# Kernel tuning notes

Hardware: AMD Instinct MI355X
Metric: run time of the kernel (lower is better)

## Reference

```python
import jax, jax.numpy as jnp
import numpy as np

N, E = 50000, 400000
NS, NV = 16, 8      # node irreps: 16x0e + 8x1o
ES, EV = 8, 8       # edge irreps: 8x0e + 8x1o
HS, HV = 32, 16     # hidden: 32x0e gated-scalar outputs, 16x1o vectors (gated by 16 extra scalars)
HT = HS + HV        # total scalar channels produced by the TP (incl. gate scalars) = 48
OS, OV = 16, 8      # output irreps: 16x0e + 8x1o


def setup_inputs() -> dict:
    key = jax.random.key(0)
    ks = jax.random.split(key, 32)
    n = lambda i, shp: jax.random.normal(ks[i], shp, dtype=jnp.float32)
    return dict(
        node_s=n(0, (N, NS)), node_v=n(1, (N, NV, 3)), pos=n(2, (N, 3)),
        edge_s=n(3, (E, ES)), edge_v=n(4, (E, EV, 3)),
        edge_index=jax.random.randint(ks[5], (2, E), 0, N, dtype=jnp.int32),
        # tp_messages stage 1: node x node -> node-sized intermediate (trilinear TP split in two)
        W1ss=n(6, (NS, NS, NS)), W1sv=n(7, (NS, NV, NV)), W1vs=n(8, (NV, NS, NV)),
        W1vvs=n(9, (NV, NV, NS)), W1vvv=n(10, (NV, NV, NV)),
        # tp_messages stage 2: intermediate x edge_attr -> hidden
        W2ss=n(11, (NS, ES, HT)), W2sv=n(12, (NS, EV, HV)), W2vs=n(13, (NV, ES, HV)),
        W2vvs=n(14, (NV, EV, HT)), W2vvv=n(15, (NV, EV, HV)),
        # lin_messages_out (per-l equivariant linear)
        Lms=n(16, (HS, OS)), Lmv=n(17, (HV, OV)),
        # tp_update: node x aggregated -> hidden
        W3ss=n(18, (NS, OS, HT)), W3sv=n(19, (NS, OV, HV)), W3vs=n(20, (NV, OS, HV)),
        W3vvs=n(21, (NV, OV, HT)), W3vvv=n(22, (NV, OV, HV)),
        # lin_update_out
        Lus=n(23, (HS, OS)), Luv=n(24, (HV, OV)),
    )


def fctp(s1, v1, s2, v2, Wss, Wsv, Wvs, Wvvs, Wvvv):
    """FullyConnectedTensorProduct restricted to l<=1 irreps.
    Paths: 0x0->0, 1x1->0 (dot), 0x1->1, 1x0->1, 1x1->1 (cross).
    Each path normalized by sqrt(fan_in); multi-path outputs by sqrt(n_paths)."""
    m1s, m2s = s1.shape[1], s2.shape[1]
    m1v, m2v = v1.shape[1], v2.shape[1]
    i2, i3 = 1.0 / np.sqrt(2.0), 1.0 / np.sqrt(3.0)
    so = jnp.einsum('ei,ej,ijk->ek', s1, s2, Wss) / np.sqrt(m1s * m2s)
    so = so + jnp.einsum('eic,ejc,ijk->ek', v1, v2, Wvvs) * (i3 / np.sqrt(m1v * m2v))
    so = so * i2
    vo = jnp.einsum('ei,ejc,ijk->ekc', s1, v2, Wsv) / np.sqrt(m1s * m2v)
    vo = vo + jnp.einsum('eic,ej,ijk->ekc', v1, s2, Wvs) / np.sqrt(m1v * m2s)
    cr = jnp.cross(v1[:, :, None, :], v2[:, None, :, :])  # [E, m1v, m2v, 3]
    vo = vo + jnp.einsum('eijc,ijk->ekc', cr, Wvvv) * (i2 / np.sqrt(m1v * m2v))
    return so, vo * i3


def gate(s, v):
    """e3nn Gate: first HS scalars silu-activated, last HV scalars sigmoid-gate the vectors."""
    hg = v.shape[1]
    return jax.nn.silu(s[:, :-hg]), v * jax.nn.sigmoid(s[:, -hg:])[:, :, None]


def lin(s, v, Ws, Wv):
    """Per-l equivariant Linear with 1/sqrt(fan_in) normalization."""
    return (s @ Ws) / np.sqrt(s.shape[1]), jnp.einsum('eic,ij->ejc', v, Wv) / np.sqrt(v.shape[1])


def reference(node_s, node_v, pos, edge_s, edge_v, edge_index,
              W1ss, W1sv, W1vs, W1vvs, W1vvv,
              W2ss, W2sv, W2vs, W2vvs, W2vvv, Lms, Lmv,
              W3ss, W3sv, W3vs, W3vvs, W3vvv, Lus, Luv):
    n_nodes = node_s.shape[0]
    row, col = edge_index[0], edge_index[1]
    # messages: trilinear TP(x_row, x_col, edge_attr) -> hidden, then gate, then linear
    ms, mv = fctp(node_s[row], node_v[row], node_s[col], node_v[col],
                  W1ss, W1sv, W1vs, W1vvs, W1vvv)
    ms, mv = fctp(ms, mv, edge_s, edge_v, W2ss, W2sv, W2vs, W2vvs, W2vvv)
    ms, mv = gate(ms, mv)
    ms, mv = lin(ms, mv, Lms, Lmv)
    # scatter-sum aggregation over destination nodes (col), dim_size = N
    agg_s = jax.ops.segment_sum(ms, col, num_segments=n_nodes)
    agg_v = jax.ops.segment_sum(mv, col, num_segments=n_nodes)
    # update: TP(node, aggregated) -> hidden, gate, linear
    us, uv = fctp(node_s, node_v, agg_s, agg_v, W3ss, W3sv, W3vs, W3vvs, W3vvv)
    us, uv = gate(us, uv)
    us, uv = lin(us, uv, Lus, Luv)
    # concatenate irreps blocks into a single [N, OS + 3*OV] feature array
    return jnp.concatenate([us, uv.reshape(n_nodes, -1)], axis=1)
```

## Files before the change

kernel.cpp:

```cpp
#include <hip/hip_runtime.h>
#include <math.h>

typedef _Float16 half8 __attribute__((ext_vector_type(8)));
typedef float floatx4 __attribute__((ext_vector_type(4)));

constexpr float C_SS16 = 0.04419417382415922f;
constexpr float C_UNI  = 0.05103103630798288f;
constexpr float C2_SS  = 0.0625f;
constexpr float C2_VS  = 0.07216878364870323f;
constexpr float C_LS   = 0.17677669529663687f;
constexpr float C_LV   = 0.25f;
constexpr float RS     = 2048.0f;
constexpr float RSI    = 1.0f / 2048.0f;

__device__ __forceinline__ void split8s(const float* p, half8& ah, half8& alS) {
#pragma unroll
    for (int j = 0; j < 8; ++j) {
        _Float16 h = (_Float16)p[j];
        ah[j] = h;
        alS[j] = (_Float16)((p[j] - (float)h) * RS);
    }
}
__device__ __forceinline__ void mfma_tri(half8 ah, half8 alS, half8 bh, half8 blS,
                                         floatx4& acc, floatx4& accR) {
    acc  = __builtin_amdgcn_mfma_f32_16x16x32_f16(ah,  bh,  acc,  0, 0, 0);
    accR = __builtin_amdgcn_mfma_f32_16x16x32_f16(alS, bh,  accR, 0, 0, 0);
    accR = __builtin_amdgcn_mfma_f32_16x16x32_f16(ah,  blS, accR, 0, 0, 0);
}

__global__ void prep_w(const float* __restrict__ W1ss, const float* __restrict__ W1sv,
                       const float* __restrict__ W1vs, const float* __restrict__ W1vvs,
                       const float* __restrict__ W1vvv,
                       const float* __restrict__ W2ss, const float* __restrict__ W2sv,
                       const float* __restrict__ W2vs, const float* __restrict__ W2vvs,
                       const float* __restrict__ W2vvv,
                       const float* __restrict__ W3ss, const float* __restrict__ W3sv,
                       const float* __restrict__ W3vs, const float* __restrict__ W3vvs,
                       const float* __restrict__ W3vvv,
                       _Float16* B1sh, _Float16* B1sl, _Float16* B1vh, _Float16* B1vl,
                       _Float16* B2sh, _Float16* B2sl, _Float16* B2vh, _Float16* B2vl,
                       _Float16* B3sh, _Float16* B3sl, _Float16* B3vh, _Float16* B3vl)
{
    const int tid = threadIdx.x;
    for (int idx = tid; idx < 10*512; idx += 256) {
        int t_k = idx >> 9, lane = (idx >> 3) & 63, j = idx & 7;
        int q = lane >> 4, n = lane & 15;
        int k = t_k*32 + q*8 + j;
        float v;
        if (k < 256) { int i = k>>4, jj = k&15; v = W1ss[(i*16+jj)*16+n] * C_SS16; }
        else { int kk = k-256; int i = kk>>3, jj = kk&7; v = W1vvs[(i*8+jj)*16+n] * C_UNI; }
        _Float16 h = (_Float16)v;
        B1sh[idx] = h; B1sl[idx] = (_Float16)((v - (float)h) * RS);
    }
    for (int idx = tid; idx < 10*512; idx += 256) {
        int t_k = idx >> 9, lane = (idx >> 3) & 63, j = idx & 7;
        int q = lane >> 4, n = lane & 15;
        int k = t_k*32 + q*8 + j;
        float v = 0.f;
        if (n < 8) {
            if (k < 128) { int i = k>>3, jj = k&7; v = W1sv[(i*8+jj)*8+n] * C_UNI; }
            else if (k < 256) { int kk = k-128; int i = kk>>4, jj = kk&15; v = W1vs[(i*16+jj)*8+n] * C_UNI; }
            else { int kk = k-256; int i = kk>>3, jj = kk&7; v = W1vvv[(i*8+jj)*8+n] * C_UNI; }
        }
        _Float16 h = (_Float16)v;
        B1vh[idx] = h; B1vl[idx] = (_Float16)((v - (float)h) * RS);
    }
    for (int idx = tid; idx < 3*6*512; idx += 256) {
        int tn = idx / 3072, t_k = (idx % 3072) >> 9, lane = (idx >> 3) & 63, j = idx & 7;
        int q = lane >> 4, n = lane & 15, col = tn*16 + n;
        int k = t_k*32 + q*8 + j;
        float v;
        if (k < 128) { int i = k>>3, jj = k&7; v = W2ss[(i*8+jj)*48+col] * C2_SS; }
        else { int kk = k-128; int i = kk>>3, jj = kk&7; v = W2vvs[(i*8+jj)*48+col] * C_UNI; }
        _Float16 h = (_Float16)v;
        B2sh[idx] = h; B2sl[idx] = (_Float16)((v - (float)h) * RS);
    }
    for (int idx = tid; idx < 8*512; idx += 256) {
        int t_k = idx >> 9, lane = (idx >> 3) & 63, j = idx & 7;
        int q = lane >> 4, n = lane & 15;
        int k = t_k*32 + q*8 + j;
        float v;
        if (k < 128) { int i = k>>3, jj = k&7; v = W2sv[(i*8+jj)*16+n] * C_UNI; }
        else if (k < 192) { int kk = k-128; int i = kk>>3, jj = kk&7; v = W2vs[(i*8+jj)*16+n] * C2_VS; }
        else { int kk = k-192; int i = kk>>3, jj = kk&7; v = W2vvv[(i*8+jj)*16+n] * C_UNI; }
        _Float16 h = (_Float16)v;
        B2vh[idx] = h; B2vl[idx] = (_Float16)((v - (float)h) * RS);
    }
    for (int idx = tid; idx < 3*10*512; idx += 256) {
        int tn = idx / 5120, rem = idx % 5120;
        int t_k = rem >> 9, lane = (rem >> 3) & 63, j = rem & 7;
        int q = lane >> 4, n = lane & 15, col = tn*16 + n;
        int k = t_k*32 + q*8 + j;
        float v;
        if (k < 256) { int i = k>>4, jj = k&15; v = W3ss[(i*16+jj)*48+col] * C_SS16; }
        else { int kk = k-256; int i = kk>>3, jj = kk&7; v = W3vvs[(i*8+jj)*48+col] * C_UNI; }
        _Float16 h = (_Float16)v;
        B3sh[idx] = h; B3sl[idx] = (_Float16)((v - (float)h) * RS);
    }
    for (int idx = tid; idx < 10*512; idx += 256) {
        int t_k = idx >> 9, lane = (idx >> 3) & 63, j = idx & 7;
        int q = lane >> 4, n = lane & 15;
        int k = t_k*32 + q*8 + j;
        float v;
        if (k < 128) { int i = k>>3, jj = k&7; v = W3sv[(i*8+jj)*16+n] * C_UNI; }
        else if (k < 256) { int kk = k-128; int i = kk>>4, jj = kk&15; v = W3vs[(i*16+jj)*16+n] * C_UNI; }
        else { int kk = k-256; int i = kk>>3, jj = kk&7; v = W3vvv[(i*8+jj)*16+n] * C_UNI; }
        _Float16 h = (_Float16)v;
        B3vh[idx] = h; B3vl[idx] = (_Float16)((v - (float)h) * RS);
    }
}

__global__ __launch_bounds__(256)
void edge_fused(const float* __restrict__ ns, const float* __restrict__ nv,
                const float* __restrict__ edge_s, const float* __restrict__ edge_v,
                const int* __restrict__ ei,
                const _Float16* __restrict__ B1sh, const _Float16* __restrict__ B1sl,
                const _Float16* __restrict__ B1vh, const _Float16* __restrict__ B1vl,
                const _Float16* __restrict__ B2sh, const _Float16* __restrict__ B2sl,
                const _Float16* __restrict__ B2vh, const _Float16* __restrict__ B2vl,
                const float* __restrict__ Lms, const float* __restrict__ Lmv,
                float* __restrict__ m2h, int E)
{
    __shared__ float mT[4][16*41];
    __shared__ float ep[4][2][16*49];
    const int lane = threadIdx.x & 63;
    const int wv = threadIdx.x >> 6;
    const int e0 = (blockIdx.x*4 + wv) * 16;
    const int q = lane >> 4, n = lane & 15;
    const int e = min(e0 + n, E - 1);
    const int qh = q >> 1, ql = q & 1;
    const int r = ei[e], c2 = ei[E + e];

    float rs_sel[8], rs4[4], rva[2][3], rvs[4][3], csh[8], cv[8][3];
#pragma unroll
    for (int t = 0; t < 8; ++t) rs_sel[t] = ns[(size_t)r*16 + 2*t + qh];
#pragma unroll
    for (int t = 0; t < 4; ++t) rs4[t] = ns[(size_t)r*16 + 4*t + q];
#pragma unroll
    for (int cc = 0; cc < 3; ++cc) {
        rva[0][cc] = nv[(size_t)r*24 + 3*q + cc];
        rva[1][cc] = nv[(size_t)r*24 + 3*(q+4) + cc];
    }
#pragma unroll
    for (int u = 0; u < 4; ++u)
#pragma unroll
        for (int cc = 0; cc < 3; ++cc) rvs[u][cc] = nv[(size_t)r*24 + 3*(2*u+qh) + cc];
    {
        const float4* p = (const float4*)(ns + (size_t)c2*16 + ql*8);
#pragma unroll
        for (int t = 0; t < 2; ++t) { float4 v = p[t]; csh[4*t]=v.x; csh[4*t+1]=v.y; csh[4*t+2]=v.z; csh[4*t+3]=v.w; }
        const float4* pv = (const float4*)(nv + (size_t)c2*24);
        float tmp[24];
#pragma unroll
        for (int t = 0; t < 6; ++t) { float4 v = pv[t]; tmp[4*t]=v.x; tmp[4*t+1]=v.y; tmp[4*t+2]=v.z; tmp[4*t+3]=v.w; }
#pragma unroll
        for (int k = 0; k < 8; ++k) { cv[k][0]=tmp[3*k]; cv[k][1]=tmp[3*k+1]; cv[k][2]=tmp[3*k+2]; }
    }

    const half8* B1sH = (const half8*)B1sh; const half8* B1sL = (const half8*)B1sl;
    const half8* B1vH = (const half8*)B1vh; const half8* B1vL = (const half8*)B1vl;

    {
        floatx4 acc = {0.f,0.f,0.f,0.f}, accR = {0.f,0.f,0.f,0.f};
#pragma unroll
        for (int t = 0; t < 10; ++t) {
            float p[8];
            if (t < 8) {
                const float m = rs_sel[t];
#pragma unroll
                for (int j = 0; j < 8; ++j) p[j] = m * csh[j];
            } else {
                const int u = t - 8;
                const float vx = rva[u][0], vy = rva[u][1], vz = rva[u][2];
#pragma unroll
                for (int j = 0; j < 8; ++j) p[j] = fmaf(vx, cv[j][0], fmaf(vy, cv[j][1], vz*cv[j][2]));
            }
            half8 ah, al; split8s(p, ah, al);
            mfma_tri(ah, al, B1sH[t*64 + lane], B1sL[t*64 + lane], acc, accR);
        }
#pragma unroll
        for (int r2 = 0; r2 < 4; ++r2)
            mT[wv][(q*4 + r2)*41 + n] = acc[r2] + accR[r2]*RSI;
    }
#pragma unroll 1
    for (int c = 0; c < 3; ++c) {
        const int c1 = (c+1)%3, c2i = (c+2)%3;
        floatx4 acc = {0.f,0.f,0.f,0.f}, accR = {0.f,0.f,0.f,0.f};
#pragma unroll
        for (int t = 0; t < 10; ++t) {
            float p[8];
            if (t < 4) {
                const float m = rs4[t];
#pragma unroll
                for (int j = 0; j < 8; ++j) p[j] = m * cv[j][c];
            } else if (t < 8) {
                const float m = rvs[t-4][c];
#pragma unroll
                for (int j = 0; j < 8; ++j) p[j] = m * csh[j];
            } else {
                const int u = t - 8;
                const float v1 = rva[u][c1], v2 = rva[u][c2i];
#pragma unroll
                for (int j = 0; j < 8; ++j) p[j] = v1*cv[j][c2i] - v2*cv[j][c1];
            }
            half8 ah, al; split8s(p, ah, al);
            mfma_tri(ah, al, B1vH[t*64 + lane], B1vL[t*64 + lane], acc, accR);
        }
        if (n < 8) {
#pragma unroll
            for (int r2 = 0; r2 < 4; ++r2)
                mT[wv][(q*4 + r2)*41 + 16 + 3*n + c] = acc[r2] + accR[r2]*RSI;
        }
    }
    __syncthreads();

    float msr[4], mva[2][3], es[8], ev[8][3];
#pragma unroll
    for (int t = 0; t < 4; ++t) msr[t] = mT[wv][n*41 + 4*t + q];
#pragma unroll
    for (int u = 0; u < 2; ++u)
#pragma unroll
        for (int cc = 0; cc < 3; ++cc) mva[u][cc] = mT[wv][n*41 + 16 + 3*(4*u+q) + cc];
    {
        const float4* p = (const float4*)(edge_s + (size_t)e*8);
#pragma unroll
        for (int t = 0; t < 2; ++t) { float4 v = p[t]; es[4*t]=v.x; es[4*t+1]=v.y; es[4*t+2]=v.z; es[4*t+3]=v.w; }
        const float4* pv = (const float4*)(edge_v + (size_t)e*24);
        float tmp[24];
#pragma unroll
        for (int t = 0; t < 6; ++t) { float4 v = pv[t]; tmp[4*t]=v.x; tmp[4*t+1]=v.y; tmp[4*t+2]=v.z; tmp[4*t+3]=v.w; }
#pragma unroll
        for (int k = 0; k < 8; ++k) { ev[k][0]=tmp[3*k]; ev[k][1]=tmp[3*k+1]; ev[k][2]=tmp[3*k+2]; }
    }

    const half8* B2sH = (const half8*)B2sh; const half8* B2sL = (const half8*)B2sl;
    const half8* B2vH = (const half8*)B2vh; const half8* B2vL = (const half8*)B2vl;

    floatx4 accs[3], accsR[3];
#pragma unroll
    for (int t = 0; t < 3; ++t) { accs[t] = (floatx4){0.f,0.f,0.f,0.f}; accsR[t] = (floatx4){0.f,0.f,0.f,0.f}; }
#pragma unroll
    for (int t = 0; t < 6; ++t) {
        float p[8];
        if (t < 4) {
            const float m = msr[t];
#pragma unroll
            for (int j = 0; j < 8; ++j) p[j] = m * es[j];
        } else {
            const int u = t - 4;
            const float vx = mva[u][0], vy = mva[u][1], vz = mva[u][2];
#pragma unroll
            for (int j = 0; j < 8; ++j) p[j] = fmaf(vx, ev[j][0], fmaf(vy, ev[j][1], vz*ev[j][2]));
        }
        half8 ah, al; split8s(p, ah, al);
#pragma unroll
        for (int tn = 0; tn < 3; ++tn)
            mfma_tri(ah, al, B2sH[(tn*6 + t)*64 + lane], B2sL[(tn*6 + t)*64 + lane], accs[tn], accsR[tn]);
    }

    float* hsL = &ep[wv][0][0];
    float* gvL = &ep[wv][1][0];
#pragma unroll
    for (int t = 0; t < 3; ++t)
#pragma unroll
        for (int r2 = 0; r2 < 4; ++r2) {
            const int row = q*4 + r2;
            const float v = accs[t][r2] + accsR[t][r2]*RSI;
            if (t < 2) hsL[row*49 + t*16 + n] = v / (1.f + __expf(-v)) * C_LS;
            else       hsL[row*49 + 32 + n] = v;
        }
    __syncthreads();

    {
        float os[4] = {0.f, 0.f, 0.f, 0.f};
#pragma unroll 4
        for (int s = 0; s < 32; ++s) {
            const float hv_ = hsL[n*49 + s];
            const float4 w = *(const float4*)(Lms + s*16 + 4*q);
            os[0] = fmaf(hv_, w.x, os[0]); os[1] = fmaf(hv_, w.y, os[1]);
            os[2] = fmaf(hv_, w.z, os[2]); os[3] = fmaf(hv_, w.w, os[3]);
        }
        if (e0 + n < E) {
#pragma unroll
            for (int u = 0; u < 4; ++u)
                m2h[(size_t)(e0 + n)*40 + 4*q + u] = os[u];
        }
    }

    floatx4 accv[3];
#pragma unroll 1
    for (int c = 0; c < 3; ++c) {
        const int c1 = (c+1)%3, c2i = (c+2)%3;
        floatx4 acc = {0.f,0.f,0.f,0.f}, accR = {0.f,0.f,0.f,0.f};
#pragma unroll
        for (int t = 0; t < 8; ++t) {
            float p[8];
            if (t < 4) {
                const float m = msr[t];
#pragma unroll
                for (int j = 0; j < 8; ++j) p[j] = m * ev[j][c];
            } else if (t < 6) {
                const float m = mva[t-4][c];
#pragma unroll
                for (int j = 0; j < 8; ++j) p[j] = m * es[j];
            } else {
                const int u = t - 6;
                const float v1 = mva[u][c1], v2 = mva[u][c2i];
#pragma unroll
                for (int j = 0; j < 8; ++j) p[j] = v1*ev[j][c2i] - v2*ev[j][c1];
            }
            half8 ah, al; split8s(p, ah, al);
            mfma_tri(ah, al, B2vH[t*64 + lane], B2vL[t*64 + lane], acc, accR);
        }
#pragma unroll
        for (int r2 = 0; r2 < 4; ++r2) acc[r2] = acc[r2] + accR[r2]*RSI;
        accv[c] = acc;
    }
#pragma unroll
    for (int r2 = 0; r2 < 4; ++r2) {
        const int row = q*4 + r2;
        const float gt = C_LV / (1.f + __expf(-hsL[row*49 + 32 + n]));
#pragma unroll
        for (int c = 0; c < 3; ++c) gvL[row*49 + c*16 + n] = accv[c][r2] * gt;
    }
    __syncthreads();

    {
        float ov[3][2] = {{0.f,0.f},{0.f,0.f},{0.f,0.f}};
#pragma unroll 4
        for (int k = 0; k < 16; ++k) {
            const float2 w = *(const float2*)(Lmv + k*8 + 2*q);
#pragma unroll
            for (int c = 0; c < 3; ++c) {
                const float gv = gvL[n*49 + c*16 + k];
                ov[c][0] = fmaf(gv, w.x, ov[c][0]);
                ov[c][1] = fmaf(gv, w.y, ov[c][1]);
            }
        }
        if (e0 + n < E) {
#pragma unroll
            for (int o2 = 0; o2 < 2; ++o2)
#pragma unroll
                for (int c = 0; c < 3; ++c)
                    m2h[(size_t)(e0 + n)*40 + 16 + 3*(2*q + o2) + c] = ov[c][o2];
        }
    }
}

__global__ void hist_k(const int* __restrict__ ei, int* __restrict__ deg, int E) {
    const int e = blockIdx.x*256 + threadIdx.x;
    if (e < E) atomicAdd(&deg[ei[E + e]], 1);
}
__global__ void scan_k(const int* __restrict__ deg, int* __restrict__ offs,
                       int* __restrict__ pos, int N) {
    __shared__ int sm[1024];
    const int t = threadIdx.x;
    const int chunk = (N + 1023) / 1024;
    const int lo = t * chunk, hi = min(lo + chunk, N);
    int s = 0;
    for (int i = lo; i < hi; ++i) s += deg[i];
    sm[t] = s; __syncthreads();
    for (int off = 1; off < 1024; off <<= 1) {
        int v = (t >= off) ? sm[t - off] : 0;
        __syncthreads();
        sm[t] += v;
        __syncthreads();
    }
    int base = sm[t] - s;
    for (int i = lo; i < hi; ++i) { offs[i] = base; pos[i] = base; base += deg[i]; }
}
__global__ void fill_k(const int* __restrict__ ei, int* __restrict__ pos,
                       int* __restrict__ order, int E) {
    const int e = blockIdx.x*256 + threadIdx.x;
    if (e < E) { int p = atomicAdd(&pos[ei[E + e]], 1); order[p] = e; }
}

__global__ __launch_bounds__(256)
void agg_k(const float* __restrict__ m2h,
           const int* __restrict__ deg, const int* __restrict__ offs,
           const int* __restrict__ order,
           float* __restrict__ agg, int N)
{
    const int n = blockIdx.x*256 + threadIdx.x;
    if (n >= N) return;
    float a[40];
#pragma unroll
    for (int u = 0; u < 40; ++u) a[u] = 0.f;
    const int cnt = deg[n], base = offs[n];
    for (int t = 0; t < cnt; ++t) {
        const int id = order[base + t];
        const float4* mp = (const float4*)(m2h + (size_t)id*40);
#pragma unroll
        for (int u = 0; u < 10; ++u) {
            float4 v = mp[u];
            a[4*u] += v.x; a[4*u+1] += v.y; a[4*u+2] += v.z; a[4*u+3] += v.w;
        }
    }
    float4* o = (float4*)(agg + (size_t)n*40);
#pragma unroll
    for (int u = 0; u < 10; ++u) o[u] = make_float4(a[4*u], a[4*u+1], a[4*u+2], a[4*u+3]);
}

__global__ __launch_bounds__(256)
void node_mfma(const float* __restrict__ ns, const float* __restrict__ nv,
               const float* __restrict__ agg,
               const _Float16* __restrict__ B3sh, const _Float16* __restrict__ B3sl,
               const _Float16* __restrict__ B3vh, const _Float16* __restrict__ B3vl,
               const float* __restrict__ Lus, const float* __restrict__ Luv,
               float* __restrict__ out, int N)
{
    __shared__ float ep[4][2][16*49];
    const int lane = threadIdx.x & 63;
    const int wv = threadIdx.x >> 6;
    const int n0 = (blockIdx.x*4 + wv) * 16;
    const int q = lane >> 4, n = lane & 15;
    const int nd = min(n0 + n, N - 1);
    const int qh = q >> 1, ql = q & 1;

    float rs_sel[8], rs4[4], rva[2][3], rvs[4][3];
#pragma unroll
    for (int t = 0; t < 8; ++t) rs_sel[t] = ns[(size_t)nd*16 + 2*t + qh];
#pragma unroll
    for (int t = 0; t < 4; ++t) rs4[t] = ns[(size_t)nd*16 + 4*t + q];
#pragma unroll
    for (int cc = 0; cc < 3; ++cc) {
        rva[0][cc] = nv[(size_t)nd*24 + 3*q + cc];
        rva[1][cc] = nv[(size_t)nd*24 + 3*(q+4) + cc];
    }
#pragma unroll
    for (int u = 0; u < 4; ++u)
#pragma unroll
        for (int cc = 0; cc < 3; ++cc) rvs[u][cc] = nv[(size_t)nd*24 + 3*(2*u+qh) + cc];
    float csh[8], cv[8][3];
    {
        const float4* p = (const float4*)(agg + (size_t)nd*40 + ql*8);
#pragma unroll
        for (int t = 0; t < 2; ++t) { float4 v = p[t]; csh[4*t]=v.x; csh[4*t+1]=v.y; csh[4*t+2]=v.z; csh[4*t+3]=v.w; }
        const float4* pv = (const float4*)(agg + (size_t)nd*40 + 16);
        float tmp[24];
#pragma unroll
        for (int t = 0; t < 6; ++t) { float4 v = pv[t]; tmp[4*t]=v.x; tmp[4*t+1]=v.y; tmp[4*t+2]=v.z; tmp[4*t+3]=v.w; }
#pragma unroll
        for (int k = 0; k < 8; ++k) { cv[k][0]=tmp[3*k]; cv[k][1]=tmp[3*k+1]; cv[k][2]=tmp[3*k+2]; }
    }

    const half8* B3sH = (const half8*)B3sh; const half8* B3sL = (const half8*)B3sl;
    const half8* B3vH = (const half8*)B3vh; const half8* B3vL = (const half8*)B3vl;

    floatx4 accs[3], accsR[3];
#pragma unroll
    for (int t = 0; t < 3; ++t) { accs[t] = (floatx4){0.f,0.f,0.f,0.f}; accsR[t] = (floatx4){0.f,0.f,0.f,0.f}; }
#pragma unroll
    for (int t = 0; t < 10; ++t) {
        float p[8];
        if (t < 8) {
            const float m = rs_sel[t];
#pragma unroll
            for (int j = 0; j < 8; ++j) p[j] = m * csh[j];
        } else {
            const int u = t - 8;
            const float vx = rva[u][0], vy = rva[u][1], vz = rva[u][2];
#pragma unroll
            for (int j = 0; j < 8; ++j) p[j] = fmaf(vx, cv[j][0], fmaf(vy, cv[j][1], vz*cv[j][2]));
        }
        half8 ah, al; split8s(p, ah, al);
#pragma unroll
        for (int tn = 0; tn < 3; ++tn)
            mfma_tri(ah, al, B3sH[(tn*10 + t)*64 + lane], B3sL[(tn*10 + t)*64 + lane], accs[tn], accsR[tn]);
    }

    float* hsL = &ep[wv][0][0];
    float* gvL = &ep[wv][1][0];
#pragma unroll
    for (int t = 0; t < 3; ++t)
#pragma unroll
        for (int r2 = 0; r2 < 4; ++r2) {
            const int row = q*4 + r2;
            const float v = accs[t][r2] + accsR[t][r2]*RSI;
            if (t < 2) hsL[row*49 + t*16 + n] = v / (1.f + __expf(-v)) * C_LS;
            else       hsL[row*49 + 32 + n] = v;
        }
    __syncthreads();

    {
        float os[4] = {0.f, 0.f, 0.f, 0.f};
#pragma unroll 4
        for (int s = 0; s < 32; ++s) {
            const float hv_ = hsL[n*49 + s];
            const float4 w = *(const float4*)(Lus + s*16 + 4*q);
            os[0] = fmaf(hv_, w.x, os[0]); os[1] = fmaf(hv_, w.y, os[1]);
            os[2] = fmaf(hv_, w.z, os[2]); os[3] = fmaf(hv_, w.w, os[3]);
        }
        if (n0 + n < N) {
#pragma unroll
            for (int u = 0; u < 4; ++u)
                out[(size_t)(n0 + n)*40 + 4*q + u] = os[u];
        }
    }

    floatx4 accv[3];
#pragma unroll 1
    for (int c = 0; c < 3; ++c) {
        const int c1 = (c+1)%3, c2i = (c+2)%3;
        floatx4 acc = {0.f,0.f,0.f,0.f}, accR = {0.f,0.f,0.f,0.f};
#pragma unroll
        for (int t = 0; t < 10; ++t) {
            float p[8];
            if (t < 4) {
                const float m = rs4[t];
#pragma unroll
                for (int j = 0; j < 8; ++j) p[j] = m * cv[j][c];
            } else if (t < 8) {
                const float m = rvs[t-4][c];
#pragma unroll
                for (int j = 0; j < 8; ++j) p[j] = m * csh[j];
            } else {
                const int u = t - 8;
                const float v1 = rva[u][c1], v2 = rva[u][c2i];
#pragma unroll
                for (int j = 0; j < 8; ++j) p[j] = v1*cv[j][c2i] - v2*cv[j][c1];
            }
            half8 ah, al; split8s(p, ah, al);
            mfma_tri(ah, al, B3vH[t*64 + lane], B3vL[t*64 + lane], acc, accR);
        }
#pragma unroll
        for (int r2 = 0; r2 < 4; ++r2) acc[r2] = acc[r2] + accR[r2]*RSI;
        accv[c] = acc;
    }
#pragma unroll
    for (int r2 = 0; r2 < 4; ++r2) {
        const int row = q*4 + r2;
        const float gt = C_LV / (1.f + __expf(-hsL[row*49 + 32 + n]));
#pragma unroll
        for (int c = 0; c < 3; ++c) gvL[row*49 + c*16 + n] = accv[c][r2] * gt;
    }
    __syncthreads();

    {
        float ov[3][2] = {{0.f,0.f},{0.f,0.f},{0.f,0.f}};
#pragma unroll 4
        for (int k = 0; k < 16; ++k) {
            const float2 w = *(const float2*)(Luv + k*8 + 2*q);
#pragma unroll
            for (int c = 0; c < 3; ++c) {
                const float gv = gvL[n*49 + c*16 + k];
                ov[c][0] = fmaf(gv, w.x, ov[c][0]);
                ov[c][1] = fmaf(gv, w.y, ov[c][1]);
            }
        }
        if (n0 + n < N) {
#pragma unroll
            for (int o2 = 0; o2 < 2; ++o2)
#pragma unroll
                for (int c = 0; c < 3; ++c)
                    out[(size_t)(n0 + n)*40 + 16 + 3*(2*q + o2) + c] = ov[c][o2];
        }
    }
}

extern "C" void kernel_launch(void* const* d_in, const int* in_sizes, int n_in,
                              void* d_out, int out_size, void* d_ws, size_t ws_size,
                              hipStream_t stream) {
    const float* node_s = (const float*)d_in[0];
    const float* node_v = (const float*)d_in[1];
    const float* edge_s = (const float*)d_in[3];
    const float* edge_v = (const float*)d_in[4];
    const int*   ei     = (const int*)d_in[5];
    const float* W1ss = (const float*)d_in[6];
    const float* W1sv = (const float*)d_in[7];
    const float* W1vs = (const float*)d_in[8];
    const float* W1vvs= (const float*)d_in[9];
    const float* W1vvv= (const float*)d_in[10];
    const float* W2ss = (const float*)d_in[11];
    const float* W2sv = (const float*)d_in[12];
    const float* W2vs = (const float*)d_in[13];
    const float* W2vvs= (const float*)d_in[14];
    const float* W2vvv= (const float*)d_in[15];
    const float* Lms  = (const float*)d_in[16];
    const float* Lmv  = (const float*)d_in[17];
    const float* W3ss = (const float*)d_in[18];
    const float* W3sv = (const float*)d_in[19];
    const float* W3vs = (const float*)d_in[20];
    const float* W3vvs= (const float*)d_in[21];
    const float* W3vvv= (const float*)d_in[22];
    const float* Lus  = (const float*)d_in[23];
    const float* Luv  = (const float*)d_in[24];

    float* out = (float*)d_out;
    const int N = in_sizes[0] / 16;
    const int E = in_sizes[5] / 2;

    _Float16* B1sh = (_Float16*)d_ws;
    _Float16* B1sl = B1sh + 5120;
    _Float16* B1vh = B1sl + 5120;
    _Float16* B1vl = B1vh + 5120;
    _Float16* B2sh = B1vl + 5120;
    _Float16* B2sl = B2sh + 9216;
    _Float16* B2vh = B2sl + 9216;
    _Float16* B2vl = B2vh + 4096;
    _Float16* B3sh = B2vl + 4096;
    _Float16* B3sl = B3sh + 15360;
    _Float16* B3vh = B3sl + 15360;
    _Float16* B3vl = B3vh + 5120;
    float* m2h = (float*)((char*)d_ws + 176128);
    float* agg = m2h + (size_t)40*E;
    int* deg   = (int*)(agg + (size_t)40*N);
    int* offs  = deg + N;
    int* pos   = offs + N;
    int* order = pos + N;

    hipMemsetAsync(deg, 0, (size_t)N * sizeof(int), stream);

    prep_w<<<1, 256, 0, stream>>>(W1ss, W1sv, W1vs, W1vvs, W1vvv,
                                  W2ss, W2sv, W2vs, W2vvs, W2vvv,
                                  W3ss, W3sv, W3vs, W3vvs, W3vvv,
                                  B1sh, B1sl, B1vh, B1vl, B2sh, B2sl, B2vh, B2vl,
                                  B3sh, B3sl, B3vh, B3vl);

    hist_k<<<(E + 255)/256, 256, 0, stream>>>(ei, deg, E);
    scan_k<<<1, 1024, 0, stream>>>(deg, offs, pos, N);
    fill_k<<<(E + 255)/256, 256, 0, stream>>>(ei, pos, order, E);

    const int tpblocks = (E + 63) / 64;
    edge_fused<<<tpblocks, 256, 0, stream>>>(
        node_s, node_v, edge_s, edge_v, ei,
        B1sh, B1sl, B1vh, B1vl, B2sh, B2sl, B2vh, B2vl,
        Lms, Lmv, m2h, E);

    agg_k<<<(N + 255)/256, 256, 0, stream>>>(m2h, deg, offs, order, agg, N);

    const int ndblocks = ((N + 15)/16 + 3) / 4;
    node_mfma<<<ndblocks, 256, 0, stream>>>(
        node_s, node_v, agg, B3sh, B3sl, B3vh, B3vl, Lus, Luv, out, N);
}
```

Baseline: 686.3 us.

## Write edge messages in destination-sorted order, drop block syncs, parallelize weight prep

Edge messages are now written straight to their rank position in destination-sorted order, so the aggregation kernel reads each node's messages contiguously instead of gathering through an order array. Block-wide __syncthreads are replaced by per-wave LDS waitcnt fences, since each wave only touches its own LDS region. LDS use is cut by aliasing buffers, the weight-prep kernel runs on 88 blocks instead of one, and the fp16 hi/lo split uses packed conversions with bit masking. The stores from the edge kernel become scattered, and the LDS fence relies on each wave's lanes staying in lockstep.

```diff
diff --git a/kernel.cpp b/kernel.cpp
--- a/kernel.cpp
+++ b/kernel.cpp
@@ -2,6 +2,7 @@
 #include <math.h>
 
 typedef _Float16 half8 __attribute__((ext_vector_type(8)));
+typedef __fp16 fp16x2 __attribute__((ext_vector_type(2)));
 typedef float floatx4 __attribute__((ext_vector_type(4)));
 
 constexpr float C_SS16 = 0.04419417382415922f;
@@ -13,12 +14,17 @@
 constexpr float RS     = 2048.0f;
 constexpr float RSI    = 1.0f / 2048.0f;
 
+#define LDS_FENCE() asm volatile("s_waitcnt lgkmcnt(0)" ::: "memory")
+
 __device__ __forceinline__ void split8s(const float* p, half8& ah, half8& alS) {
 #pragma unroll
-    for (int j = 0; j < 8; ++j) {
-        _Float16 h = (_Float16)p[j];
-        ah[j] = h;
-        alS[j] = (_Float16)((p[j] - (float)h) * RS);
+    for (int j = 0; j < 8; j += 2) {
+        fp16x2 h = __builtin_amdgcn_cvt_pkrtz(p[j], p[j+1]);
+        const float b0 = __uint_as_float(__float_as_uint(p[j])   & 0xFFFFE000u);
+        const float b1 = __uint_as_float(__float_as_uint(p[j+1]) & 0xFFFFE000u);
+        fp16x2 l = __builtin_amdgcn_cvt_pkrtz((p[j] - b0) * RS, (p[j+1] - b1) * RS);
+        ah[j] = (_Float16)h[0]; ah[j+1] = (_Float16)h[1];
+        alS[j] = (_Float16)l[0]; alS[j+1] = (_Float16)l[1];
     }
 }
 __device__ __forceinline__ void mfma_tri(half8 ah, half8 alS, half8 bh, half8 blS,
@@ -41,8 +47,9 @@
                        _Float16* B2sh, _Float16* B2sl, _Float16* B2vh, _Float16* B2vl,
                        _Float16* B3sh, _Float16* B3sl, _Float16* B3vh, _Float16* B3vl)
 {
-    const int tid = threadIdx.x;
-    for (int idx = tid; idx < 10*512; idx += 256) {
+    const int t0 = blockIdx.x*256 + threadIdx.x;
+    const int gs = gridDim.x*256;
+    for (int idx = t0; idx < 10*512; idx += gs) {
         int t_k = idx >> 9, lane = (idx >> 3) & 63, j = idx & 7;
         int q = lane >> 4, n = lane & 15;
         int k = t_k*32 + q*8 + j;
@@ -52,7 +59,7 @@
         _Float16 h = (_Float16)v;
         B1sh[idx] = h; B1sl[idx] = (_Float16)((v - (float)h) * RS);
     }
-    for (int idx = tid; idx < 10*512; idx += 256) {
+    for (int idx = t0; idx < 10*512; idx += gs) {
         int t_k = idx >> 9, lane = (idx >> 3) & 63, j = idx & 7;
         int q = lane >> 4, n = lane & 15;
         int k = t_k*32 + q*8 + j;
@@ -65,7 +72,7 @@
         _Float16 h = (_Float16)v;
         B1vh[idx] = h; B1vl[idx] = (_Float16)((v - (float)h) * RS);
     }
-    for (int idx = tid; idx < 3*6*512; idx += 256) {
+    for (int idx = t0; idx < 3*6*512; idx += gs) {
         int tn = idx / 3072, t_k = (idx % 3072) >> 9, lane = (idx >> 3) & 63, j = idx & 7;
         int q = lane >> 4, n = lane & 15, col = tn*16 + n;
         int k = t_k*32 + q*8 + j;
@@ -75,7 +82,7 @@
         _Float16 h = (_Float16)v;
         B2sh[idx] = h; B2sl[idx] = (_Float16)((v - (float)h) * RS);
     }
-    for (int idx = tid; idx < 8*512; idx += 256) {
+    for (int idx = t0; idx < 8*512; idx += gs) {
         int t_k = idx >> 9, lane = (idx >> 3) & 63, j = idx & 7;
         int q = lane >> 4, n = lane & 15;
         int k = t_k*32 + q*8 + j;
@@ -86,7 +93,7 @@
         _Float16 h = (_Float16)v;
         B2vh[idx] = h; B2vl[idx] = (_Float16)((v - (float)h) * RS);
     }
-    for (int idx = tid; idx < 3*10*512; idx += 256) {
+    for (int idx = t0; idx < 3*10*512; idx += gs) {
         int tn = idx / 5120, rem = idx % 5120;
         int t_k = rem >> 9, lane = (rem >> 3) & 63, j = rem & 7;
         int q = lane >> 4, n = lane & 15, col = tn*16 + n;
@@ -97,7 +104,7 @@
         _Float16 h = (_Float16)v;
         B3sh[idx] = h; B3sl[idx] = (_Float16)((v - (float)h) * RS);
     }
-    for (int idx = tid; idx < 10*512; idx += 256) {
+    for (int idx = t0; idx < 10*512; idx += gs) {
         int t_k = idx >> 9, lane = (idx >> 3) & 63, j = idx & 7;
         int q = lane >> 4, n = lane & 15;
         int k = t_k*32 + q*8 + j;
@@ -113,7 +120,7 @@
 __global__ __launch_bounds__(256)
 void edge_fused(const float* __restrict__ ns, const float* __restrict__ nv,
                 const float* __restrict__ edge_s, const float* __restrict__ edge_v,
-                const int* __restrict__ ei,
+                const int* __restrict__ ei, const int* __restrict__ rank,
                 const _Float16* __restrict__ B1sh, const _Float16* __restrict__ B1sl,
                 const _Float16* __restrict__ B1vh, const _Float16* __restrict__ B1vl,
                 const _Float16* __restrict__ B2sh, const _Float16* __restrict__ B2sl,
@@ -121,8 +128,7 @@
                 const float* __restrict__ Lms, const float* __restrict__ Lmv,
                 float* __restrict__ m2h, int E)
 {
-    __shared__ float mT[4][16*41];
-    __shared__ float ep[4][2][16*49];
+    __shared__ float buf[4][1568];
     const int lane = threadIdx.x & 63;
     const int wv = threadIdx.x >> 6;
     const int e0 = (blockIdx.x*4 + wv) * 16;
@@ -130,6 +136,10 @@
     const int e = min(e0 + n, E - 1);
     const int qh = q >> 1, ql = q & 1;
     const int r = ei[e], c2 = ei[E + e];
+    const int slot = rank[e];
+    float* const mTl = &buf[wv][0];
+    float* const hsL = &buf[wv][0];
+    float* const gvL = &buf[wv][784];
 
     float rs_sel[8], rs4[4], rva[2][3], rvs[4][3], csh[8], cv[8][3];
 #pragma unroll
@@ -180,7 +190,7 @@
         }
 #pragma unroll
         for (int r2 = 0; r2 < 4; ++r2)
-            mT[wv][(q*4 + r2)*41 + n] = acc[r2] + accR[r2]*RSI;
+            mTl[(q*4 + r2)*41 + n] = acc[r2] + accR[r2]*RSI;
     }
 #pragma unroll 1
     for (int c = 0; c < 3; ++c) {
@@ -209,18 +219,18 @@
         if (n < 8) {
 #pragma unroll
             for (int r2 = 0; r2 < 4; ++r2)
-                mT[wv][(q*4 + r2)*41 + 16 + 3*n + c] = acc[r2] + accR[r2]*RSI;
-        }
-    }
-    __syncthreads();
+                mTl[(q*4 + r2)*41 + 16 + 3*n + c] = acc[r2] + accR[r2]*RSI;
+        }
+    }
+    LDS_FENCE();
 
     float msr[4], mva[2][3], es[8], ev[8][3];
 #pragma unroll
-    for (int t = 0; t < 4; ++t) msr[t] = mT[wv][n*41 + 4*t + q];
+    for (int t = 0; t < 4; ++t) msr[t] = mTl[n*41 + 4*t + q];
 #pragma unroll
     for (int u = 0; u < 2; ++u)
 #pragma unroll
-        for (int cc = 0; cc < 3; ++cc) mva[u][cc] = mT[wv][n*41 + 16 + 3*(4*u+q) + cc];
+        for (int cc = 0; cc < 3; ++cc) mva[u][cc] = mTl[n*41 + 16 + 3*(4*u+q) + cc];
     {
         const float4* p = (const float4*)(edge_s + (size_t)e*8);
 #pragma unroll
@@ -258,8 +268,7 @@
             mfma_tri(ah, al, B2sH[(tn*6 + t)*64 + lane], B2sL[(tn*6 + t)*64 + lane], accs[tn], accsR[tn]);
     }
 
-    float* hsL = &ep[wv][0][0];
-    float* gvL = &ep[wv][1][0];
+    LDS_FENCE();
 #pragma unroll
     for (int t = 0; t < 3; ++t)
 #pragma unroll
@@ -269,7 +278,7 @@
             if (t < 2) hsL[row*49 + t*16 + n] = v / (1.f + __expf(-v)) * C_LS;
             else       hsL[row*49 + 32 + n] = v;
         }
-    __syncthreads();
+    LDS_FENCE();
 
     {
         float os[4] = {0.f, 0.f, 0.f, 0.f};
@@ -283,7 +292,7 @@
         if (e0 + n < E) {
 #pragma unroll
             for (int u = 0; u < 4; ++u)
-                m2h[(size_t)(e0 + n)*40 + 4*q + u] = os[u];
+                m2h[(size_t)slot*40 + 4*q + u] = os[u];
         }
     }
 
@@ -323,7 +332,7 @@
 #pragma unroll
         for (int c = 0; c < 3; ++c) gvL[row*49 + c*16 + n] = accv[c][r2] * gt;
     }
-    __syncthreads();
+    LDS_FENCE();
 
     {
         float ov[3][2] = {{0.f,0.f},{0.f,0.f},{0.f,0.f}};
@@ -342,7 +351,7 @@
             for (int o2 = 0; o2 < 2; ++o2)
 #pragma unroll
                 for (int c = 0; c < 3; ++c)
-                    m2h[(size_t)(e0 + n)*40 + 16 + 3*(2*q + o2) + c] = ov[c][o2];
+                    m2h[(size_t)slot*40 + 16 + 3*(2*q + o2) + c] = ov[c][o2];
         }
     }
 }
@@ -370,15 +379,14 @@
     for (int i = lo; i < hi; ++i) { offs[i] = base; pos[i] = base; base += deg[i]; }
 }
 __global__ void fill_k(const int* __restrict__ ei, int* __restrict__ pos,
-                       int* __restrict__ order, int E) {
+                       int* __restrict__ rank, int E) {
     const int e = blockIdx.x*256 + threadIdx.x;
-    if (e < E) { int p = atomicAdd(&pos[ei[E + e]], 1); order[p] = e; }
+    if (e < E) { int p = atomicAdd(&pos[ei[E + e]], 1); rank[e] = p; }
 }
 
 __global__ __launch_bounds__(256)
 void agg_k(const float* __restrict__ m2h,
            const int* __restrict__ deg, const int* __restrict__ offs,
-           const int* __restrict__ order,
            float* __restrict__ agg, int N)
 {
     const int n = blockIdx.x*256 + threadIdx.x;
@@ -386,13 +394,12 @@
     float a[40];
 #pragma unroll
     for (int u = 0; u < 40; ++u) a[u] = 0.f;
-    const int cnt = deg[n], base = offs[n];
+    const int cnt = deg[n];
+    const float4* mp = (const float4*)(m2h + (size_t)offs[n]*40);
     for (int t = 0; t < cnt; ++t) {
-        const int id = order[base + t];
-        const float4* mp = (const float4*)(m2h + (size_t)id*40);
 #pragma unroll
         for (int u = 0; u < 10; ++u) {
-            float4 v = mp[u];
+            float4 v = mp[(size_t)t*10 + u];
             a[4*u] += v.x; a[4*u+1] += v.y; a[4*u+2] += v.z; a[4*u+3] += v.w;
         }
     }
@@ -480,7 +487,7 @@
             if (t < 2) hsL[row*49 + t*16 + n] = v / (1.f + __expf(-v)) * C_LS;
             else       hsL[row*49 + 32 + n] = v;
         }
-    __syncthreads();
+    LDS_FENCE();
 
     {
         float os[4] = {0.f, 0.f, 0.f, 0.f};
@@ -534,7 +541,7 @@
 #pragma unroll
         for (int c = 0; c < 3; ++c) gvL[row*49 + c*16 + n] = accv[c][r2] * gt;
     }
-    __syncthreads();
+    LDS_FENCE();
 
     {
         float ov[3][2] = {{0.f,0.f},{0.f,0.f},{0.f,0.f}};
@@ -607,27 +614,27 @@
     int* deg   = (int*)(agg + (size_t)40*N);
     int* offs  = deg + N;
     int* pos   = offs + N;
-    int* order = pos + N;
+    int* rank  = pos + N;
 
     hipMemsetAsync(deg, 0, (size_t)N * sizeof(int), stream);
 
-    prep_w<<<1, 256, 0, stream>>>(W1ss, W1sv, W1vs, W1vvs, W1vvv,
-                                  W2ss, W2sv, W2vs, W2vvs, W2vvv,
-                                  W3ss, W3sv, W3vs, W3vvs, W3vvv,
-                                  B1sh, B1sl, B1vh, B1vl, B2sh, B2sl, B2vh, B2vl,
-                                  B3sh, B3sl, B3vh, B3vl);
+    prep_w<<<88, 256, 0, stream>>>(W1ss, W1sv, W1vs, W1vvs, W1vvv,
+                                   W2ss, W2sv, W2vs, W2vvs, W2vvv,
+                                   W3ss, W3sv, W3vs, W3vvs, W3vvv,
+                                   B1sh, B1sl, B1vh, B1vl, B2sh, B2sl, B2vh, B2vl,
+                                   B3sh, B3sl, B3vh, B3vl);
 
     hist_k<<<(E + 255)/256, 256, 0, stream>>>(ei, deg, E);
     scan_k<<<1, 1024, 0, stream>>>(deg, offs, pos, N);
-    fill_k<<<(E + 255)/256, 256, 0, stream>>>(ei, pos, order, E);
+    fill_k<<<(E + 255)/256, 256, 0, stream>>>(ei, pos, rank, E);
 
     const int tpblocks = (E + 63) / 64;
     edge_fused<<<tpblocks, 256, 0, stream>>>(
-        node_s, node_v, edge_s, edge_v, ei,
+        node_s, node_v, edge_s, edge_v, ei, rank,
         B1sh, B1sl, B1vh, B1vl, B2sh, B2sl, B2vh, B2vl,
         Lms, Lmv, m2h, E);
 
-    agg_k<<<(N + 255)/256, 256, 0, stream>>>(m2h, deg, offs, order, agg, N);
+    agg_k<<<(N + 255)/256, 256, 0, stream>>>(m2h, deg, offs, agg, N);
 
     const int ndblocks = ((N + 15)/16 + 3) / 4;
     node_mfma<<<ndblocks, 256, 0, stream>>>(
```

After: 643.8 us. -6.2%, faster.
